# Performance work log

Hardware: AMD Instinct MI355X
Metric: run time of the kernel (lower is better)

Reference implementation:

```python
import jax, jax.numpy as jnp
import numpy as np

MARGIN = 0.2
EPS = 1e-6


def setup_inputs() -> dict:
    key = jax.random.key(0)
    k1, k2 = jax.random.split(key)
    B, C = 8192, 1024
    z_label = jax.random.randint(k1, (B,), 0, 256, dtype=jnp.int64 if jax.config.jax_enable_x64 else jnp.int32)
    z_idx = jnp.arange(B, dtype=z_label.dtype)
    z = jax.random.normal(k2, (B, C), dtype=jnp.float32)
    return {"z_label": z_label, "z_idx": z_idx, "z": z}


def reference(z_label, z_idx, z):
    B = z.shape[0]
    k = max(2, int(B * 0.01))  # static: labels overwritten if batch has a single unique label
    all_same = jnp.all(z_label == z_label[0])
    z_label = jnp.where(all_same & (jnp.arange(B) < k), -1, z_label)

    # Vectorized triplet mining (replaces per-sample Python loop):
    # positive: first j with same label, different sample idx; negative: first j with different label.
    label_eq = z_label[:, None] == z_label[None, :]            # [B, B]
    pos_mask = label_eq & (z_idx[:, None] != z_idx[None, :])   # [B, B]
    neg_mask = ~label_eq                                       # [B, B]
    pos_idx = jnp.argmax(pos_mask, axis=1)  # first True (torch.where(...)[0][0])
    neg_idx = jnp.argmax(neg_mask, axis=1)
    valid = pos_mask.any(axis=1) & neg_mask.any(axis=1)        # [B]

    # TripletMarginLoss (p=2, swap=False): d(x,y) = ||x - y + eps||_2
    a, p_emb, n_emb = z, z[pos_idx], z[neg_idx]
    d_ap = jnp.sqrt(jnp.sum((a - p_emb + EPS) ** 2, axis=1))
    d_an = jnp.sqrt(jnp.sum((a - n_emb + EPS) ** 2, axis=1))
    per = jnp.maximum(d_ap - d_an + MARGIN, 0.0)               # [B]

    n_valid = valid.sum()
    vf = valid.astype(per.dtype)
    loss = jnp.where(n_valid > 0,
                     jnp.sum(per * vf) / jnp.maximum(n_valid, 1).astype(per.dtype),
                     jnp.array(0.0, per.dtype))
    return loss
```

## Files before the change

### kernel.cpp

```cpp
#include <hip/hip_runtime.h>

#define MARGIN 0.2f
#define EPSC 1e-6f

__device__ inline void acc8(const float4& av, const float4& pv, const float4& nv,
                            float& sap, float& san) {
    float d;
    d = av.x - pv.x + EPSC; sap += d * d;
    d = av.y - pv.y + EPSC; sap += d * d;
    d = av.z - pv.z + EPSC; sap += d * d;
    d = av.w - pv.w + EPSC; sap += d * d;
    d = av.x - nv.x + EPSC; san += d * d;
    d = av.y - nv.y + EPSC; san += d * d;
    d = av.z - nv.z + EPSC; san += d * d;
    d = av.w - nv.w + EPSC; san += d * d;
}

__device__ inline void scan4(const int4& lj, const int4& xj, int li, int myidx,
                             int j0, int& pos, int& neg) {
    if (pos < 0) {
        int m = ((lj.x == li && xj.x != myidx) ? 1 : 0)
              | ((lj.y == li && xj.y != myidx) ? 2 : 0)
              | ((lj.z == li && xj.z != myidx) ? 4 : 0)
              | ((lj.w == li && xj.w != myidx) ? 8 : 0);
        unsigned long long b = __ballot(m != 0);
        if (b) {
            int L  = __ffsll(b) - 1;
            int mL = __shfl(m, L, 64);
            pos = j0 + L * 4 + (__ffs(mL) - 1);
        }
    }
    if (neg < 0) {
        int m = ((lj.x != li) ? 1 : 0) | ((lj.y != li) ? 2 : 0)
              | ((lj.z != li) ? 4 : 0) | ((lj.w != li) ? 8 : 0);
        unsigned long long b = __ballot(m != 0);
        if (b) {
            int L  = __ffsll(b) - 1;
            int mL = __shfl(m, L, 64);
            neg = j0 + L * 4 + (__ffs(mL) - 1);
        }
    }
}

__device__ inline void mine_row_64(const int* __restrict__ label,
                                   const int* __restrict__ zidx, int B, int lane,
                                   int li, int myidx, int& pos, int& neg) {
    pos = -1; neg = -1;
    for (int j0 = 0; j0 < B && (pos < 0 || neg < 0); j0 += 64) {
        int j = j0 + lane;
        bool inb = j < B;
        int lj = 0, xj = 0;
        if (inb) { lj = label[j]; xj = zidx[j]; }
        unsigned long long pb = __ballot(inb && lj == li && xj != myidx);
        unsigned long long nb = __ballot(inb && lj != li);
        if (pos < 0 && pb) pos = j0 + __ffsll(pb) - 1;
        if (neg < 0 && nb) neg = j0 + __ffsll(nb) - 1;
    }
}

__device__ inline void mine_allsame(const int* __restrict__ zidx, int B, int lane,
                                    int i, int myidx, int& pos, int& neg) {
    int k = B / 100; if (k < 2) k = 2;
    int kk = k < B ? k : B;
    int lo, hi;
    if (i < kk) { lo = 0;  hi = kk; neg = (kk < B) ? kk : -1; }
    else        { lo = kk; hi = B;  neg = 0; }
    pos = -1;
    for (int j0 = lo; j0 < hi && pos < 0; j0 += 64) {
        int j = j0 + lane;
        bool ok = (j < hi) && (zidx[j] != myidx);
        unsigned long long b = __ballot(ok);
        if (b) pos = j0 + __ffsll(b) - 1;
    }
}

__global__ __launch_bounds__(256) void mine_kernel(
    const int* __restrict__ label, const int* __restrict__ zidx,
    int B, int2* __restrict__ pn)
{
    const int wave = threadIdx.x >> 6;
    const int lane = threadIdx.x & 63;
    const int i = blockIdx.x * 4 + wave;
    if (i >= B) return;

    const int li = label[i];
    const int myidx = zidx[i];
    int pos = -1, neg = -1;

    if ((B & 255) == 0) {
        for (int j0 = 0; j0 < B && (pos < 0 || neg < 0); j0 += 256) {
            const int base = j0 + lane * 4;
            int4 lj = *(const int4*)(label + base);
            int4 xj = *(const int4*)(zidx + base);
            scan4(lj, xj, li, myidx, j0, pos, neg);
        }
    } else {
        mine_row_64(label, zidx, B, lane, li, myidx, pos, neg);
    }
    if (neg < 0)
        mine_allsame(zidx, B, lane, i, myidx, pos, neg);

    if (lane == 0) pn[i] = make_int2(pos, neg);
}

__device__ inline void row_generic(const float* __restrict__ z, int i, int pi,
                                   int ni, int C, int lane,
                                   float& lsum, float& lcnt, bool valid) {
    const float4* a = (const float4*)(z + (size_t)i  * C) + lane;
    const float4* p = (const float4*)(z + (size_t)pi * C) + lane;
    const float4* n = (const float4*)(z + (size_t)ni * C) + lane;
    float sap = 0.f, san = 0.f;
    const int nk = C >> 8;
    for (int kk = 0; kk < nk; ++kk)
        acc8(a[kk * 64], p[kk * 64], n[kk * 64], sap, san);
    for (int c = (nk << 8) + lane; c < C; c += 64) {
        float av = z[(size_t)i  * C + c];
        float pv = z[(size_t)pi * C + c];
        float nv = z[(size_t)ni * C + c];
        float d = av - pv + EPSC; sap += d * d;
        d = av - nv + EPSC; san += d * d;
    }
    for (int off = 32; off; off >>= 1) {
        sap += __shfl_xor(sap, off, 64);
        san += __shfl_xor(san, off, 64);
    }
    if (lane == 0 && valid) {
        lsum += fmaxf(sqrtf(sap) - sqrtf(san) + MARGIN, 0.f);
        lcnt += 1.f;
    }
}

__global__ __launch_bounds__(256) void dist_kernel(
    const float* __restrict__ z, const int2* __restrict__ pn,
    int B, int C, float2* __restrict__ g_part)
{
    const int wave = threadIdx.x >> 6;
    const int lane = threadIdx.x & 63;
    const int ia = blockIdx.x * 8 + wave * 2;
    const int ib = ia + 1;
    const bool hasA = ia < B, hasB = ib < B;

    float lsum = 0.f, lcnt = 0.f;

    int2 pnA = hasA ? pn[ia] : make_int2(0, 0);
    int2 pnB = hasB ? pn[ib] : make_int2(0, 0);

    if (C == 1024 && hasA && hasB) {
        const int piA = pnA.x < 0 ? 0 : pnA.x;
        const int niA = pnA.y < 0 ? 0 : pnA.y;
        const int piB = pnB.x < 0 ? 0 : pnB.x;
        const int niB = pnB.y < 0 ? 0 : pnB.y;
        const float4* aA = (const float4*)(z + (size_t)ia  * 1024) + lane;
        const float4* pA = (const float4*)(z + (size_t)piA * 1024) + lane;
        const float4* nA = (const float4*)(z + (size_t)niA * 1024) + lane;
        const float4* aB = (const float4*)(z + (size_t)ib  * 1024) + lane;
        const float4* pB = (const float4*)(z + (size_t)piB * 1024) + lane;
        const float4* nB = (const float4*)(z + (size_t)niB * 1024) + lane;

        float4 A0 = aA[0], A1 = aA[64], A2 = aA[128], A3 = aA[192];
        float4 PA0 = pA[0], PA1 = pA[64], PA2 = pA[128], PA3 = pA[192];
        float4 NA0 = nA[0], NA1 = nA[64], NA2 = nA[128], NA3 = nA[192];
        float4 B0 = aB[0], B1 = aB[64], B2 = aB[128], B3 = aB[192];
        float4 PB0 = pB[0], PB1 = pB[64], PB2 = pB[128], PB3 = pB[192];
        float4 NB0 = nB[0], NB1 = nB[64], NB2 = nB[128], NB3 = nB[192];

        float sap = 0.f, san = 0.f;
        acc8(A0, PA0, NA0, sap, san); acc8(A1, PA1, NA1, sap, san);
        acc8(A2, PA2, NA2, sap, san); acc8(A3, PA3, NA3, sap, san);
        for (int off = 32; off; off >>= 1) {
            sap += __shfl_xor(sap, off, 64);
            san += __shfl_xor(san, off, 64);
        }
        if (lane == 0 && pnA.x >= 0 && pnA.y >= 0) {
            lsum += fmaxf(sqrtf(sap) - sqrtf(san) + MARGIN, 0.f);
            lcnt += 1.f;
        }

        sap = 0.f; san = 0.f;
        acc8(B0, PB0, NB0, sap, san); acc8(B1, PB1, NB1, sap, san);
        acc8(B2, PB2, NB2, sap, san); acc8(B3, PB3, NB3, sap, san);
        for (int off = 32; off; off >>= 1) {
            sap += __shfl_xor(sap, off, 64);
            san += __shfl_xor(san, off, 64);
        }
        if (lane == 0 && pnB.x >= 0 && pnB.y >= 0) {
            lsum += fmaxf(sqrtf(sap) - sqrtf(san) + MARGIN, 0.f);
            lcnt += 1.f;
        }
    } else {
        if (hasA)
            row_generic(z, ia, pnA.x < 0 ? 0 : pnA.x, pnA.y < 0 ? 0 : pnA.y,
                        C, lane, lsum, lcnt, pnA.x >= 0 && pnA.y >= 0);
        if (hasB)
            row_generic(z, ib, pnB.x < 0 ? 0 : pnB.x, pnB.y < 0 ? 0 : pnB.y,
                        C, lane, lsum, lcnt, pnB.x >= 0 && pnB.y >= 0);
    }

    __shared__ float s_sum[4], s_cnt[4];
    if (lane == 0) { s_sum[wave] = lsum; s_cnt[wave] = lcnt; }
    __syncthreads();
    if (threadIdx.x == 0) {
        float bs = 0.f, bc = 0.f;
        for (int w = 0; w < 4; ++w) { bs += s_sum[w]; bc += s_cnt[w]; }
        g_part[blockIdx.x] = make_float2(bs, bc);
    }
}

__global__ __launch_bounds__(1024) void final_kernel(
    const float2* __restrict__ g_part, int nb, float* __restrict__ out)
{
    const int t = threadIdx.x;
    float s = 0.f, c = 0.f;
    for (int idx = t; idx < nb; idx += blockDim.x) {
        float2 v = g_part[idx];
        s += v.x; c += v.y;
    }
    for (int off = 32; off; off >>= 1) {
        s += __shfl_xor(s, off, 64);
        c += __shfl_xor(c, off, 64);
    }
    __shared__ float s_s[16], s_c[16];
    const int wave = t >> 6, lane = t & 63;
    if (lane == 0) { s_s[wave] = s; s_c[wave] = c; }
    __syncthreads();
    if (t == 0) {
        float ts = 0.f, tc = 0.f;
        const int nw = blockDim.x >> 6;
        for (int w = 0; w < nw; ++w) { ts += s_s[w]; tc += s_c[w]; }
        out[0] = (tc > 0.f) ? ts / tc : 0.f;
    }
}

extern "C" void kernel_launch(void* const* d_in, const int* in_sizes, int n_in,
                              void* d_out, int out_size, void* d_ws, size_t ws_size,
                              hipStream_t stream) {
    const int*   z_label = (const int*)d_in[0];
    const int*   z_idx   = (const int*)d_in[1];
    const float* z       = (const float*)d_in[2];
    const int B = in_sizes[0];
    const int C = in_sizes[2] / B;
    float* out = (float*)d_out;

    const int nblk = (B + 7) / 8;
    float2* g_part = (float2*)d_ws;
    size_t pn_off = ((size_t)nblk * sizeof(float2) + 255) & ~(size_t)255;
    int2* pn = (int2*)((char*)d_ws + pn_off);

    mine_kernel<<<(B + 3) / 4, 256, 0, stream>>>(z_label, z_idx, B, pn);
    dist_kernel<<<nblk, 256, 0, stream>>>(z, pn, B, C, g_part);
    final_kernel<<<1, 1024, 0, stream>>>(g_part, nblk, out);
}
```

Before: 84.95 us.

## Fuse mining, distance and final reduction into one kernel with last-block reduce

```diff
diff --git a/kernel.cpp b/kernel.cpp
--- a/kernel.cpp
+++ b/kernel.cpp
@@ -2,6 +2,8 @@
 
 #define MARGIN 0.2f
 #define EPSC 1e-6f
+
+typedef unsigned long long ull;
 
 __device__ inline void acc8(const float4& av, const float4& pv, const float4& nv,
                             float& sap, float& san) {
@@ -72,35 +74,6 @@
         unsigned long long b = __ballot(ok);
         if (b) pos = j0 + __ffsll(b) - 1;
     }
-}
-
-__global__ __launch_bounds__(256) void mine_kernel(
-    const int* __restrict__ label, const int* __restrict__ zidx,
-    int B, int2* __restrict__ pn)
-{
-    const int wave = threadIdx.x >> 6;
-    const int lane = threadIdx.x & 63;
-    const int i = blockIdx.x * 4 + wave;
-    if (i >= B) return;
-
-    const int li = label[i];
-    const int myidx = zidx[i];
-    int pos = -1, neg = -1;
-
-    if ((B & 255) == 0) {
-        for (int j0 = 0; j0 < B && (pos < 0 || neg < 0); j0 += 256) {
-            const int base = j0 + lane * 4;
-            int4 lj = *(const int4*)(label + base);
-            int4 xj = *(const int4*)(zidx + base);
-            scan4(lj, xj, li, myidx, j0, pos, neg);
-        }
-    } else {
-        mine_row_64(label, zidx, B, lane, li, myidx, pos, neg);
-    }
-    if (neg < 0)
-        mine_allsame(zidx, B, lane, i, myidx, pos, neg);
-
-    if (lane == 0) pn[i] = make_int2(pos, neg);
 }
 
 __device__ inline void row_generic(const float* __restrict__ z, int i, int pi,
@@ -130,37 +103,67 @@
     }
 }
 
-__global__ __launch_bounds__(256) void dist_kernel(
-    const float* __restrict__ z, const int2* __restrict__ pn,
-    int B, int C, float2* __restrict__ g_part)
+__global__ __launch_bounds__(256) void triplet_kernel(
+    const float* __restrict__ z, const int* __restrict__ label,
+    const int* __restrict__ zidx, int B, int C,
+    float2* __restrict__ g_part, unsigned* __restrict__ counter,
+    float* __restrict__ out, int nblk)
 {
     const int wave = threadIdx.x >> 6;
     const int lane = threadIdx.x & 63;
     const int ia = blockIdx.x * 8 + wave * 2;
     const int ib = ia + 1;
     const bool hasA = ia < B, hasB = ib < B;
+    const bool fast = (C == 1024) && hasA && hasB;
 
     float lsum = 0.f, lcnt = 0.f;
 
-    int2 pnA = hasA ? pn[ia] : make_int2(0, 0);
-    int2 pnB = hasB ? pn[ib] : make_int2(0, 0);
-
-    if (C == 1024 && hasA && hasB) {
-        const int piA = pnA.x < 0 ? 0 : pnA.x;
-        const int niA = pnA.y < 0 ? 0 : pnA.y;
-        const int piB = pnB.x < 0 ? 0 : pnB.x;
-        const int niB = pnB.y < 0 ? 0 : pnB.y;
-        const float4* aA = (const float4*)(z + (size_t)ia  * 1024) + lane;
+    int liA = 0, idxA = 0, liB = 0, idxB = 0;
+    if (hasA) { liA = label[ia]; idxA = zidx[ia]; }
+    if (hasB) { liB = label[ib]; idxB = zidx[ib]; }
+
+    float4 A0, A1, A2, A3, B0, B1, B2, B3;
+    if (fast) {
+        const float4* aA = (const float4*)(z + (size_t)ia * 1024) + lane;
+        const float4* aB = (const float4*)(z + (size_t)ib * 1024) + lane;
+        A0 = aA[0]; A1 = aA[64]; A2 = aA[128]; A3 = aA[192];
+        B0 = aB[0]; B1 = aB[64]; B2 = aB[128]; B3 = aB[192];
+    }
+
+    int posA = -1, negA = -1, posB = -1, negB = -1;
+    if (hasA) {
+        if ((B & 255) == 0) {
+            if (!hasB) { posB = 0; negB = 0; }
+            for (int j0 = 0; j0 < B && (posA < 0 || negA < 0 || posB < 0 || negB < 0);
+                 j0 += 256) {
+                const int base = j0 + lane * 4;
+                int4 lj = *(const int4*)(label + base);
+                int4 xj = *(const int4*)(zidx + base);
+                scan4(lj, xj, liA, idxA, j0, posA, negA);
+                if (hasB) scan4(lj, xj, liB, idxB, j0, posB, negB);
+            }
+        } else {
+            mine_row_64(label, zidx, B, lane, liA, idxA, posA, negA);
+            if (hasB) mine_row_64(label, zidx, B, lane, liB, idxB, posB, negB);
+        }
+        if (negA < 0) {
+            mine_allsame(zidx, B, lane, ia, idxA, posA, negA);
+            if (hasB) mine_allsame(zidx, B, lane, ib, idxB, posB, negB);
+        }
+    }
+
+    if (fast) {
+        const int piA = posA < 0 ? 0 : posA;
+        const int niA = negA < 0 ? 0 : negA;
+        const int piB = posB < 0 ? 0 : posB;
+        const int niB = negB < 0 ? 0 : negB;
         const float4* pA = (const float4*)(z + (size_t)piA * 1024) + lane;
         const float4* nA = (const float4*)(z + (size_t)niA * 1024) + lane;
-        const float4* aB = (const float4*)(z + (size_t)ib  * 1024) + lane;
         const float4* pB = (const float4*)(z + (size_t)piB * 1024) + lane;
         const float4* nB = (const float4*)(z + (size_t)niB * 1024) + lane;
 
-        float4 A0 = aA[0], A1 = aA[64], A2 = aA[128], A3 = aA[192];
         float4 PA0 = pA[0], PA1 = pA[64], PA2 = pA[128], PA3 = pA[192];
         float4 NA0 = nA[0], NA1 = nA[64], NA2 = nA[128], NA3 = nA[192];
-        float4 B0 = aB[0], B1 = aB[64], B2 = aB[128], B3 = aB[192];
         float4 PB0 = pB[0], PB1 = pB[64], PB2 = pB[128], PB3 = pB[192];
         float4 NB0 = nB[0], NB1 = nB[64], NB2 = nB[128], NB3 = nB[192];
 
@@ -171,7 +174,7 @@
             sap += __shfl_xor(sap, off, 64);
             san += __shfl_xor(san, off, 64);
         }
-        if (lane == 0 && pnA.x >= 0 && pnA.y >= 0) {
+        if (lane == 0 && posA >= 0 && negA >= 0) {
             lsum += fmaxf(sqrtf(sap) - sqrtf(san) + MARGIN, 0.f);
             lcnt += 1.f;
         }
@@ -183,50 +186,59 @@
             sap += __shfl_xor(sap, off, 64);
             san += __shfl_xor(san, off, 64);
         }
-        if (lane == 0 && pnB.x >= 0 && pnB.y >= 0) {
+        if (lane == 0 && posB >= 0 && negB >= 0) {
             lsum += fmaxf(sqrtf(sap) - sqrtf(san) + MARGIN, 0.f);
             lcnt += 1.f;
         }
     } else {
         if (hasA)
-            row_generic(z, ia, pnA.x < 0 ? 0 : pnA.x, pnA.y < 0 ? 0 : pnA.y,
-                        C, lane, lsum, lcnt, pnA.x >= 0 && pnA.y >= 0);
+            row_generic(z, ia, posA < 0 ? 0 : posA, negA < 0 ? 0 : negA,
+                        C, lane, lsum, lcnt, posA >= 0 && negA >= 0);
         if (hasB)
-            row_generic(z, ib, pnB.x < 0 ? 0 : pnB.x, pnB.y < 0 ? 0 : pnB.y,
-                        C, lane, lsum, lcnt, pnB.x >= 0 && pnB.y >= 0);
+            row_generic(z, ib, posB < 0 ? 0 : posB, negB < 0 ? 0 : negB,
+                        C, lane, lsum, lcnt, posB >= 0 && negB >= 0);
     }
 
     __shared__ float s_sum[4], s_cnt[4];
+    __shared__ int s_won;
     if (lane == 0) { s_sum[wave] = lsum; s_cnt[wave] = lcnt; }
     __syncthreads();
     if (threadIdx.x == 0) {
         float bs = 0.f, bc = 0.f;
         for (int w = 0; w < 4; ++w) { bs += s_sum[w]; bc += s_cnt[w]; }
-        g_part[blockIdx.x] = make_float2(bs, bc);
-    }
-}
-
-__global__ __launch_bounds__(1024) void final_kernel(
-    const float2* __restrict__ g_part, int nb, float* __restrict__ out)
-{
+        float2 v = make_float2(bs, bc);
+        ull u; __builtin_memcpy(&u, &v, 8);
+        __hip_atomic_store((ull*)&g_part[blockIdx.x], u,
+                           __ATOMIC_RELEASE, __HIP_MEMORY_SCOPE_AGENT);
+        __threadfence();
+        unsigned old = __hip_atomic_fetch_add(counter, 1u,
+                           __ATOMIC_ACQ_REL, __HIP_MEMORY_SCOPE_AGENT);
+        s_won = (old == (unsigned)(nblk - 1)) ? 1 : 0;
+    }
+    __syncthreads();
+    if (!s_won) return;
+
     const int t = threadIdx.x;
-    float s = 0.f, c = 0.f;
-    for (int idx = t; idx < nb; idx += blockDim.x) {
-        float2 v = g_part[idx];
-        s += v.x; c += v.y;
-    }
-    for (int off = 32; off; off >>= 1) {
-        s += __shfl_xor(s, off, 64);
-        c += __shfl_xor(c, off, 64);
-    }
     __shared__ float s_s[16], s_c[16];
-    const int wave = t >> 6, lane = t & 63;
-    if (lane == 0) { s_s[wave] = s; s_c[wave] = c; }
+    for (int q = 0; q < 4; ++q) {
+        const int vt = t + 256 * q;
+        float s = 0.f, c = 0.f;
+        for (int idx = vt; idx < nblk; idx += 1024) {
+            ull u = __hip_atomic_load((const ull*)&g_part[idx],
+                                      __ATOMIC_RELAXED, __HIP_MEMORY_SCOPE_AGENT);
+            float2 v; __builtin_memcpy(&v, &u, 8);
+            s += v.x; c += v.y;
+        }
+        for (int off = 32; off; off >>= 1) {
+            s += __shfl_xor(s, off, 64);
+            c += __shfl_xor(c, off, 64);
+        }
+        if (lane == 0) { s_s[vt >> 6] = s; s_c[vt >> 6] = c; }
+    }
     __syncthreads();
     if (t == 0) {
         float ts = 0.f, tc = 0.f;
-        const int nw = blockDim.x >> 6;
-        for (int w = 0; w < nw; ++w) { ts += s_s[w]; tc += s_c[w]; }
+        for (int w = 0; w < 16; ++w) { ts += s_s[w]; tc += s_c[w]; }
         out[0] = (tc > 0.f) ? ts / tc : 0.f;
     }
 }
@@ -242,11 +254,10 @@
     float* out = (float*)d_out;
 
     const int nblk = (B + 7) / 8;
-    float2* g_part = (float2*)d_ws;
-    size_t pn_off = ((size_t)nblk * sizeof(float2) + 255) & ~(size_t)255;
-    int2* pn = (int2*)((char*)d_ws + pn_off);
-
-    mine_kernel<<<(B + 3) / 4, 256, 0, stream>>>(z_label, z_idx, B, pn);
-    dist_kernel<<<nblk, 256, 0, stream>>>(z, pn, B, C, g_part);
-    final_kernel<<<1, 1024, 0, stream>>>(g_part, nblk, out);
-}
+    unsigned* counter = (unsigned*)d_ws;
+    float2* g_part = (float2*)((char*)d_ws + 256);
+
+    hipMemsetAsync(d_ws, 0, 4, stream);
+    triplet_kernel<<<nblk, 256, 0, stream>>>(z, z_label, z_idx, B, C,
+                                             g_part, counter, out, nblk);
+}
```

Measured after the change: 126.5 us. 1.49x slower.

## Fuse triplet mining and distance computation into one kernel

Applied to the files above, without the earlier changes.

```diff
diff --git a/kernel.cpp b/kernel.cpp
--- a/kernel.cpp
+++ b/kernel.cpp
@@ -72,35 +72,6 @@
         unsigned long long b = __ballot(ok);
         if (b) pos = j0 + __ffsll(b) - 1;
     }
-}
-
-__global__ __launch_bounds__(256) void mine_kernel(
-    const int* __restrict__ label, const int* __restrict__ zidx,
-    int B, int2* __restrict__ pn)
-{
-    const int wave = threadIdx.x >> 6;
-    const int lane = threadIdx.x & 63;
-    const int i = blockIdx.x * 4 + wave;
-    if (i >= B) return;
-
-    const int li = label[i];
-    const int myidx = zidx[i];
-    int pos = -1, neg = -1;
-
-    if ((B & 255) == 0) {
-        for (int j0 = 0; j0 < B && (pos < 0 || neg < 0); j0 += 256) {
-            const int base = j0 + lane * 4;
-            int4 lj = *(const int4*)(label + base);
-            int4 xj = *(const int4*)(zidx + base);
-            scan4(lj, xj, li, myidx, j0, pos, neg);
-        }
-    } else {
-        mine_row_64(label, zidx, B, lane, li, myidx, pos, neg);
-    }
-    if (neg < 0)
-        mine_allsame(zidx, B, lane, i, myidx, pos, neg);
-
-    if (lane == 0) pn[i] = make_int2(pos, neg);
 }
 
 __device__ inline void row_generic(const float* __restrict__ z, int i, int pi,
@@ -130,78 +101,75 @@
     }
 }
 
-__global__ __launch_bounds__(256) void dist_kernel(
-    const float* __restrict__ z, const int2* __restrict__ pn,
-    int B, int C, float2* __restrict__ g_part)
+__global__ __launch_bounds__(512) void triplet_kernel(
+    const float* __restrict__ z, const int* __restrict__ label,
+    const int* __restrict__ zidx, int B, int C, float2* __restrict__ g_part)
 {
     const int wave = threadIdx.x >> 6;
     const int lane = threadIdx.x & 63;
-    const int ia = blockIdx.x * 8 + wave * 2;
-    const int ib = ia + 1;
-    const bool hasA = ia < B, hasB = ib < B;
+    const int i = blockIdx.x * 8 + wave;
+    const bool hasR = i < B;
+    const bool fast = (C == 1024) && hasR;
 
     float lsum = 0.f, lcnt = 0.f;
 
-    int2 pnA = hasA ? pn[ia] : make_int2(0, 0);
-    int2 pnB = hasB ? pn[ib] : make_int2(0, 0);
-
-    if (C == 1024 && hasA && hasB) {
-        const int piA = pnA.x < 0 ? 0 : pnA.x;
-        const int niA = pnA.y < 0 ? 0 : pnA.y;
-        const int piB = pnB.x < 0 ? 0 : pnB.x;
-        const int niB = pnB.y < 0 ? 0 : pnB.y;
-        const float4* aA = (const float4*)(z + (size_t)ia  * 1024) + lane;
-        const float4* pA = (const float4*)(z + (size_t)piA * 1024) + lane;
-        const float4* nA = (const float4*)(z + (size_t)niA * 1024) + lane;
-        const float4* aB = (const float4*)(z + (size_t)ib  * 1024) + lane;
-        const float4* pB = (const float4*)(z + (size_t)piB * 1024) + lane;
-        const float4* nB = (const float4*)(z + (size_t)niB * 1024) + lane;
-
-        float4 A0 = aA[0], A1 = aA[64], A2 = aA[128], A3 = aA[192];
-        float4 PA0 = pA[0], PA1 = pA[64], PA2 = pA[128], PA3 = pA[192];
-        float4 NA0 = nA[0], NA1 = nA[64], NA2 = nA[128], NA3 = nA[192];
-        float4 B0 = aB[0], B1 = aB[64], B2 = aB[128], B3 = aB[192];
-        float4 PB0 = pB[0], PB1 = pB[64], PB2 = pB[128], PB3 = pB[192];
-        float4 NB0 = nB[0], NB1 = nB[64], NB2 = nB[128], NB3 = nB[192];
-
+    int li = 0, myidx = 0;
+    if (hasR) { li = label[i]; myidx = zidx[i]; }
+
+    float4 A0, A1, A2, A3;
+    if (fast) {
+        const float4* a = (const float4*)(z + (size_t)i * 1024) + lane;
+        A0 = a[0]; A1 = a[64]; A2 = a[128]; A3 = a[192];
+    }
+
+    int pos = -1, neg = -1;
+    if (hasR) {
+        if ((B & 255) == 0) {
+            for (int j0 = 0; j0 < B && (pos < 0 || neg < 0); j0 += 256) {
+                const int base = j0 + lane * 4;
+                int4 lj = *(const int4*)(label + base);
+                int4 xj = *(const int4*)(zidx + base);
+                scan4(lj, xj, li, myidx, j0, pos, neg);
+            }
+        } else {
+            mine_row_64(label, zidx, B, lane, li, myidx, pos, neg);
+        }
+        if (neg < 0)
+            mine_allsame(zidx, B, lane, i, myidx, pos, neg);
+    }
+
+    if (fast) {
+        const int pi = pos < 0 ? 0 : pos;
+        const int ni = neg < 0 ? 0 : neg;
+        const float4* p = (const float4*)(z + (size_t)pi * 1024) + lane;
+        const float4* n = (const float4*)(z + (size_t)ni * 1024) + lane;
+        float4 P0 = p[0], P1 = p[64], P2 = p[128], P3 = p[192];
+        float4 N0 = n[0], N1 = n[64], N2 = n[128], N3 = n[192];
         float sap = 0.f, san = 0.f;
-        acc8(A0, PA0, NA0, sap, san); acc8(A1, PA1, NA1, sap, san);
-        acc8(A2, PA2, NA2, sap, san); acc8(A3, PA3, NA3, sap, san);
+        acc8(A0, P0, N0, sap, san); acc8(A1, P1, N1, sap, san);
+        acc8(A2, P2, N2, sap, san); acc8(A3, P3, N3, sap, san);
         for (int off = 32; off; off >>= 1) {
             sap += __shfl_xor(sap, off, 64);
             san += __shfl_xor(san, off, 64);
         }
-        if (lane == 0 && pnA.x >= 0 && pnA.y >= 0) {
+        if (lane == 0 && pos >= 0 && neg >= 0) {
             lsum += fmaxf(sqrtf(sap) - sqrtf(san) + MARGIN, 0.f);
             lcnt += 1.f;
         }
-
-        sap = 0.f; san = 0.f;
-        acc8(B0, PB0, NB0, sap, san); acc8(B1, PB1, NB1, sap, san);
-        acc8(B2, PB2, NB2, sap, san); acc8(B3, PB3, NB3, sap, san);
-        for (int off = 32; off; off >>= 1) {
-            sap += __shfl_xor(sap, off, 64);
-            san += __shfl_xor(san, off, 64);
-        }
-        if (lane == 0 && pnB.x >= 0 && pnB.y >= 0) {
-            lsum += fmaxf(sqrtf(sap) - sqrtf(san) + MARGIN, 0.f);
-            lcnt += 1.f;
-        }
-    } else {
-        if (hasA)
-            row_generic(z, ia, pnA.x < 0 ? 0 : pnA.x, pnA.y < 0 ? 0 : pnA.y,
-                        C, lane, lsum, lcnt, pnA.x >= 0 && pnA.y >= 0);
-        if (hasB)
-            row_generic(z, ib, pnB.x < 0 ? 0 : pnB.x, pnB.y < 0 ? 0 : pnB.y,
-                        C, lane, lsum, lcnt, pnB.x >= 0 && pnB.y >= 0);
-    }
-
-    __shared__ float s_sum[4], s_cnt[4];
+    } else if (hasR) {
+        row_generic(z, i, pos < 0 ? 0 : pos, neg < 0 ? 0 : neg,
+                    C, lane, lsum, lcnt, pos >= 0 && neg >= 0);
+    }
+
+    __shared__ float s_sum[8], s_cnt[8];
     if (lane == 0) { s_sum[wave] = lsum; s_cnt[wave] = lcnt; }
     __syncthreads();
     if (threadIdx.x == 0) {
         float bs = 0.f, bc = 0.f;
-        for (int w = 0; w < 4; ++w) { bs += s_sum[w]; bc += s_cnt[w]; }
+        for (int w = 0; w < 4; ++w) {
+            bs += (s_sum[2 * w] + s_sum[2 * w + 1]);
+            bc += (s_cnt[2 * w] + s_cnt[2 * w + 1]);
+        }
         g_part[blockIdx.x] = make_float2(bs, bc);
     }
 }
@@ -243,10 +211,7 @@
 
     const int nblk = (B + 7) / 8;
     float2* g_part = (float2*)d_ws;
-    size_t pn_off = ((size_t)nblk * sizeof(float2) + 255) & ~(size_t)255;
-    int2* pn = (int2*)((char*)d_ws + pn_off);
-
-    mine_kernel<<<(B + 3) / 4, 256, 0, stream>>>(z_label, z_idx, B, pn);
-    dist_kernel<<<nblk, 256, 0, stream>>>(z, pn, B, C, g_part);
+
+    triplet_kernel<<<nblk, 512, 0, stream>>>(z, z_label, z_idx, B, C, g_part);
     final_kernel<<<1, 1024, 0, stream>>>(g_part, nblk, out);
 }
```

Measured after the change: 84.22 us (median of 2 runs). No clear change (-0.9%).
